# Kernel tuning notes

Measured on AMD Instinct MI355X. Metric: run time of the kernel, lower is better.

The kernel has to match this reference:

```python
import jax, jax.numpy as jnp
import numpy as np

H = 64          # hidden_size
FF = 36         # MLP hidden
B, W, S = 512, 8, 200


def setup_inputs() -> dict:
    key = jax.random.key(0)
    ks = jax.random.split(key, 8)
    query = jax.random.normal(ks[0], (B, H), dtype=jnp.float32)
    k = jax.random.normal(ks[1], (B, W, S, H), dtype=jnp.float32)
    mask = jax.random.randint(ks[2], (B, W, S, 1), 0, 2).astype(bool)
    # MLP params: Linear(4H -> 36), PReLU(scalar), Linear(36 -> 1)
    lim1 = 1.0 / np.sqrt(4 * H)
    W1 = jax.random.uniform(ks[3], (FF, 4 * H), jnp.float32, -lim1, lim1)
    b1 = jax.random.uniform(ks[4], (FF,), jnp.float32, -lim1, lim1)
    prelu_a = jnp.float32(0.25)
    lim2 = 1.0 / np.sqrt(FF)
    W2 = jax.random.uniform(ks[5], (1, FF), jnp.float32, -lim2, lim2)
    b2 = jax.random.uniform(ks[6], (1,), jnp.float32, -lim2, lim2)
    return {"query": query, "key": k, "W1": W1, "b1": b1,
            "prelu_a": prelu_a, "W2": W2, "b2": b2, "mask": mask}


def reference(query, key, W1, b1, prelu_a, W2, b2, mask):
    # broadcast query to (B, W, S, H)
    q = jnp.broadcast_to(query[:, None, None, :], key.shape)
    feat = jnp.concatenate([q, key, q - key, q * key], axis=-1)  # (B,W,S,4H)
    h = jnp.einsum('bwsf,of->bwso', feat, W1) + b1               # (B,W,S,36)
    h = jnp.where(h >= 0, h, prelu_a * h)                        # PReLU
    score = jnp.einsum('bwso,uo->bwsu', h, W2) + b2              # (B,W,S,1)
    # weighted_att=True: mask with -1e4 then softmax over seq_len
    score = jnp.where(mask, jnp.float32(-10000.0), score)
    score = jax.nn.softmax(score, axis=2)
    out = (key * score).sum(axis=2)                              # (B,W,H)
    return out
```

## Files before the change

kernel.cpp:

```cpp
#include <hip/hip_runtime.h>
#include <math.h>


#define BB   512
#define WW   8
#define SS   200
#define HH   64
#define FFN  36

typedef __attribute__((ext_vector_type(8))) short short8;
typedef __attribute__((ext_vector_type(4))) float f32x4;

__device__ __forceinline__ unsigned short f2bf(float x) {
    union { float f; unsigned u; } v; v.f = x;
    unsigned r = v.u + 0x7fffu + ((v.u >> 16) & 1u);
    return (unsigned short)(r >> 16);
}
__device__ __forceinline__ float bf2f(unsigned short h) {
    union { unsigned u; float f; } v; v.u = ((unsigned)h) << 16;
    return v.f;
}

__global__ __launch_bounds__(256)
void precompute_c(const float* __restrict__ query,
                  const float* __restrict__ W1,
                  const float* __restrict__ b1,
                  unsigned short* __restrict__ c_hi_g,
                  float* __restrict__ A_g)
{
    __shared__ float q_s[HH];
    const int b = blockIdx.x, tid = threadIdx.x;
    if (tid < HH) q_s[tid] = query[b * HH + tid];
    __syncthreads();
    for (int idx = tid; idx < 48 * HH; idx += 256) {
        int o = idx >> 6, h = idx & 63;
        float c = 0.0f;
        if (o < FFN) {
            const float* w = W1 + o * 4 * HH;
            c = w[HH + h] - w[2 * HH + h] + w[3 * HH + h] * q_s[h];
        }
        c_hi_g[(size_t)b * 48 * HH + idx] = f2bf(c);
    }
    if (tid < 48) {
        float a = 0.0f;
        if (tid < FFN) {
            const float* w = W1 + tid * 4 * HH;
            a = b1[tid];
            #pragma unroll 8
            for (int h = 0; h < HH; ++h) a += (w[h] + w[2 * HH + h]) * q_s[h];
        }
        A_g[b * 48 + tid] = a;
    }
}

__global__ __launch_bounds__(256, 4)
void twb_main(const float* __restrict__ key,
              const unsigned short* __restrict__ c_hi_g,
              const float* __restrict__ A_g,
              const float* __restrict__ prelu_a,
              const float* __restrict__ W2,
              const int*   __restrict__ mask,
              float*       __restrict__ out)
{
    __shared__ float scores[208];
    __shared__ float wl[208];
    __shared__ float red[8];
    __shared__ float4 part4[256];

    const int tid  = threadIdx.x;
    const int bw   = blockIdx.x;
    const int b    = bw >> 3;
    const int lane = tid & 63, q = lane >> 4, n = lane & 15, wid = tid >> 6;

    const float* kg = key + (size_t)bw * (SS * HH);
    const unsigned short* cb = c_hi_g + (size_t)b * 48 * HH;

    short8 Bf[3][2];
    float  Ao[3], w2o[3];
    #pragma unroll
    for (int ot = 0; ot < 3; ++ot) {
        const int o = ot * 16 + n;
        #pragma unroll
        for (int ks = 0; ks < 2; ++ks)
            Bf[ot][ks] = *(const short8*)(cb + (size_t)o * HH + ks * 32 + q * 8);
        Ao[ot]  = A_g[b * 48 + o];
        w2o[ot] = (o < FFN) ? W2[o] : 0.0f;
    }
    int mv = 1;
    if (tid < SS) mv = mask[bw * SS + tid];
    const float pa = prelu_a[0];

    for (int st = wid; st < 13; st += 4) {
        const int s = st * 16 + n;
        short8 Ah[2], Al[2];
        if (s < SS) {
            #pragma unroll
            for (int ks = 0; ks < 2; ++ks) {
                const float* p = kg + s * HH + ks * 32 + q * 8;
                const float4 v0 = *(const float4*)p;
                const float4 v1 = *(const float4*)(p + 4);
                const float vv[8] = {v0.x, v0.y, v0.z, v0.w,
                                     v1.x, v1.y, v1.z, v1.w};
                #pragma unroll
                for (int j = 0; j < 8; ++j) {
                    const unsigned short hi = f2bf(vv[j]);
                    Ah[ks][j] = (short)hi;
                    Al[ks][j] = (short)f2bf(vv[j] - bf2f(hi));
                }
            }
        } else {
            #pragma unroll
            for (int ks = 0; ks < 2; ++ks)
                #pragma unroll
                for (int j = 0; j < 8; ++j) { Ah[ks][j] = 0; Al[ks][j] = 0; }
        }
        float contrib[4] = {0.f, 0.f, 0.f, 0.f};
        #pragma unroll
        for (int ot = 0; ot < 3; ++ot) {
            f32x4 acc = {0.f, 0.f, 0.f, 0.f};
            acc = __builtin_amdgcn_mfma_f32_16x16x32_bf16(Ah[0], Bf[ot][0], acc, 0, 0, 0);
            acc = __builtin_amdgcn_mfma_f32_16x16x32_bf16(Al[0], Bf[ot][0], acc, 0, 0, 0);
            acc = __builtin_amdgcn_mfma_f32_16x16x32_bf16(Ah[1], Bf[ot][1], acc, 0, 0, 0);
            acc = __builtin_amdgcn_mfma_f32_16x16x32_bf16(Al[1], Bf[ot][1], acc, 0, 0, 0);
            #pragma unroll
            for (int r = 0; r < 4; ++r) {
                float hv = acc[r] + Ao[ot];
                hv = (hv >= 0.0f) ? hv : pa * hv;
                contrib[r] += w2o[ot] * hv;
            }
        }
        #pragma unroll
        for (int m = 1; m <= 8; m <<= 1)
            #pragma unroll
            for (int r = 0; r < 4; ++r)
                contrib[r] += __shfl_xor(contrib[r], m, 64);
        if (n == 0) {
            #pragma unroll
            for (int r = 0; r < 4; ++r) {
                const int s2 = st * 16 + q * 4 + r;
                if (s2 < SS) scores[s2] = contrib[r];
            }
        }
    }
    __syncthreads();

    float msc = -3.0e38f;
    if (tid < SS)
        msc = mv ? -10000.0f : scores[tid];
    float mx = msc;
    #pragma unroll
    for (int off = 32; off > 0; off >>= 1)
        mx = fmaxf(mx, __shfl_xor(mx, off, 64));
    if (lane == 0) red[wid] = mx;
    __syncthreads();
    const float M = fmaxf(fmaxf(red[0], red[1]), fmaxf(red[2], red[3]));
    float e = (tid < SS) ? __expf(msc - M) : 0.0f;
    float ssum = e;
    #pragma unroll
    for (int off = 32; off > 0; off >>= 1)
        ssum += __shfl_xor(ssum, off, 64);
    if (lane == 0) red[4 + wid] = ssum;
    __syncthreads();
    const float total = red[4] + red[5] + red[6] + red[7];
    if (tid < SS) wl[tid] = e / total;
    __syncthreads();

    {
        const int r0 = tid >> 4;
        const int h4 = (tid & 15) * 4;
        float4 acc2 = {0.f, 0.f, 0.f, 0.f};
        for (int s = r0; s < SS; s += 16) {
            const float4 kv = *(const float4*)(kg + s * HH + h4);
            const float w = wl[s];
            acc2.x += kv.x * w; acc2.y += kv.y * w;
            acc2.z += kv.z * w; acc2.w += kv.w * w;
        }
        part4[tid] = acc2;
    }
    __syncthreads();
    if (tid < HH) {
        const int hg = tid >> 2, c = tid & 3;
        float r = 0.0f;
        #pragma unroll
        for (int row = 0; row < 16; ++row)
            r += ((const float*)&part4[row * 16 + hg])[c];
        out[(size_t)bw * HH + tid] = r;
    }
}

#define PADQ 17
__global__ __launch_bounds__(256, 2)
void twb_fallback(const float* __restrict__ query,
                  const float* __restrict__ key,
                  const float* __restrict__ W1,
                  const float* __restrict__ b1,
                  const float* __restrict__ prelu_a,
                  const float* __restrict__ W2,
                  const float* __restrict__ b2,
                  const int*   __restrict__ mask,
                  float*       __restrict__ out)
{
    __shared__ float q_s[HH];
    __shared__ float c_s[FFN * HH];
    __shared__ float A_s[FFN];
    __shared__ float W2_s[FFN];
    __shared__ float k_s[SS * PADQ * 4];
    __shared__ float wl[256];
    __shared__ float red[8];
    __shared__ float part[4 * 64];

    const int tid = threadIdx.x;
    const int bw  = blockIdx.x;
    const int b   = bw >> 3;

    if (tid < HH)  q_s[tid]  = query[b * HH + tid];
    if (tid < FFN) W2_s[tid] = W2[tid];
    __syncthreads();

    const float4* gk4 = (const float4*)(key + (size_t)bw * (SS * HH));
    float4* kl4 = (float4*)k_s;
    for (int i = tid; i < (SS * HH) / 4; i += 256) {
        float4 v = gk4[i];
        kl4[(i >> 4) * PADQ + (i & 15)] = v;
    }
    for (int idx = tid; idx < FFN * HH; idx += 256) {
        int o = idx >> 6, h = idx & 63;
        const float* w = W1 + o * (4 * HH);
        c_s[idx] = w[HH + h] - w[2 * HH + h] + w[3 * HH + h] * q_s[h];
    }
    if (tid < FFN) {
        const float* w = W1 + tid * (4 * HH);
        float a = b1[tid];
        for (int h = 0; h < HH; ++h) a += (w[h] + w[2 * HH + h]) * q_s[h];
        A_s[tid] = a;
    }
    __syncthreads();

    const float pa  = prelu_a[0];
    const float bb2 = b2[0];
    float msc = -3.0e38f;
    if (tid < SS) {
        float acc[FFN];
        #pragma unroll
        for (int o = 0; o < FFN; ++o) acc[o] = A_s[o];
        const float4* c4 = (const float4*)c_s;
        const float4* k4 = (const float4*)k_s;
        const int rowbase = tid * PADQ;
        for (int ch = 0; ch < 4; ++ch) {
            float4 kv0 = k4[rowbase + ch * 4 + 0];
            float4 kv1 = k4[rowbase + ch * 4 + 1];
            float4 kv2 = k4[rowbase + ch * 4 + 2];
            float4 kv3 = k4[rowbase + ch * 4 + 3];
            #pragma unroll
            for (int o = 0; o < FFN; ++o) {
                float4 c0 = c4[o * 16 + ch * 4 + 0];
                float4 c1 = c4[o * 16 + ch * 4 + 1];
                float4 c2 = c4[o * 16 + ch * 4 + 2];
                float4 c3 = c4[o * 16 + ch * 4 + 3];
                float a = acc[o];
                a += c0.x * kv0.x + c0.y * kv0.y + c0.z * kv0.z + c0.w * kv0.w;
                a += c1.x * kv1.x + c1.y * kv1.y + c1.z * kv1.z + c1.w * kv1.w;
                a += c2.x * kv2.x + c2.y * kv2.y + c2.z * kv2.z + c2.w * kv2.w;
                a += c3.x * kv3.x + c3.y * kv3.y + c3.z * kv3.z + c3.w * kv3.w;
                acc[o] = a;
            }
        }
        float sc = bb2;
        #pragma unroll
        for (int o = 0; o < FFN; ++o) {
            float a = acc[o];
            a = (a >= 0.0f) ? a : pa * a;
            sc += W2_s[o] * a;
        }
        msc = mask[bw * SS + tid] ? -10000.0f : sc;
    }

    float mx = msc;
    #pragma unroll
    for (int off = 32; off > 0; off >>= 1)
        mx = fmaxf(mx, __shfl_xor(mx, off, 64));
    const int wid = tid >> 6;
    if ((tid & 63) == 0) red[wid] = mx;
    __syncthreads();
    const float M = fmaxf(fmaxf(red[0], red[1]), fmaxf(red[2], red[3]));
    float e = (tid < SS) ? __expf(msc - M) : 0.0f;
    float ssum = e;
    #pragma unroll
    for (int off = 32; off > 0; off >>= 1)
        ssum += __shfl_xor(ssum, off, 64);
    if ((tid & 63) == 0) red[4 + wid] = ssum;
    __syncthreads();
    const float total = red[4] + red[5] + red[6] + red[7];
    if (tid < SS) wl[tid] = e / total;
    __syncthreads();

    const int wv = tid >> 6, h = tid & 63;
    float p = 0.0f;
    for (int s = wv * 50; s < wv * 50 + 50; ++s)
        p += k_s[s * (PADQ * 4) + h] * wl[s];
    part[wv * 64 + h] = p;
    __syncthreads();
    if (tid < 64) {
        float r = part[tid] + part[64 + tid] + part[128 + tid] + part[192 + tid];
        out[(size_t)bw * HH + tid] = r;
    }
}

extern "C" void kernel_launch(void* const* d_in, const int* in_sizes, int n_in,
                              void* d_out, int out_size, void* d_ws, size_t ws_size,
                              hipStream_t stream) {
    const float* query   = (const float*)d_in[0];
    const float* key     = (const float*)d_in[1];
    const float* W1      = (const float*)d_in[2];
    const float* b1      = (const float*)d_in[3];
    const float* prelu_a = (const float*)d_in[4];
    const float* W2      = (const float*)d_in[5];
    const float* b2      = (const float*)d_in[6];
    const int*   mask    = (const int*)d_in[7];
    float* out = (float*)d_out;

    const size_t c_bytes = (size_t)BB * 48 * HH * sizeof(unsigned short);
    const size_t a_bytes = (size_t)BB * 48 * sizeof(float);
    if (ws_size >= c_bytes + a_bytes) {
        unsigned short* c_hi_g = (unsigned short*)d_ws;
        float* A_g = (float*)((char*)d_ws + c_bytes);
        precompute_c<<<BB, 256, 0, stream>>>(query, W1, b1, c_hi_g, A_g);
        twb_main<<<BB * WW, 256, 0, stream>>>(key, c_hi_g, A_g, prelu_a,
                                              W2, mask, out);
    } else {
        twb_fallback<<<BB * WW, 256, 0, stream>>>(query, key, W1, b1, prelu_a,
                                                  W2, b2, mask, out);
    }
}
```

Baseline: 323.7 us.

## Fuse precompute into main kernel and keep key tile in registers for both passes

Folds the per-batch precompute of the c and A vectors into the main kernel, staging them in shared memory, so there is one launch and no workspace round-trip. The key tile is loaded once into registers up front and reused for both the MLP scoring and the weighted sum, replacing the second global read of key. Each of the 8 blocks sharing a batch now recomputes c and A redundantly, register pressure rises, and launch bounds drop to 2 blocks per SM. The fallback kernel is removed and bf16 conversion now uses the HIP intrinsic.

```diff
diff --git a/kernel.cpp b/kernel.cpp
--- a/kernel.cpp
+++ b/kernel.cpp
@@ -1,4 +1,5 @@
 #include <hip/hip_runtime.h>
+#include <hip/hip_bf16.h>
 #include <math.h>
 
 
@@ -7,100 +8,118 @@
 #define SS   200
 #define HH   64
 #define FFN  36
+#define SCST 72
 
 typedef __attribute__((ext_vector_type(8))) short short8;
 typedef __attribute__((ext_vector_type(4))) float f32x4;
 
 __device__ __forceinline__ unsigned short f2bf(float x) {
-    union { float f; unsigned u; } v; v.f = x;
-    unsigned r = v.u + 0x7fffu + ((v.u >> 16) & 1u);
-    return (unsigned short)(r >> 16);
+    __hip_bfloat16 h = __float2bfloat16(x);
+    union { __hip_bfloat16 b; unsigned short u; } c; c.b = h;
+    return c.u;
 }
 __device__ __forceinline__ float bf2f(unsigned short h) {
     union { unsigned u; float f; } v; v.u = ((unsigned)h) << 16;
     return v.f;
 }
 
-__global__ __launch_bounds__(256)
-void precompute_c(const float* __restrict__ query,
-                  const float* __restrict__ W1,
-                  const float* __restrict__ b1,
-                  unsigned short* __restrict__ c_hi_g,
-                  float* __restrict__ A_g)
+__global__ __launch_bounds__(256, 2)
+void twb_fused(const float* __restrict__ query,
+               const float* __restrict__ key,
+               const float* __restrict__ W1,
+               const float* __restrict__ b1,
+               const float* __restrict__ prelu_a,
+               const float* __restrict__ W2,
+               const int*   __restrict__ mask,
+               float*       __restrict__ out)
 {
     __shared__ float q_s[HH];
-    const int b = blockIdx.x, tid = threadIdx.x;
+    __shared__ unsigned short c_s[48 * SCST];
+    __shared__ float A_s[48], W2_s[48];
+    __shared__ float partA[144];
+    __shared__ float scores[208];
+    __shared__ float wl[208];
+    __shared__ float red[8];
+    __shared__ float part[4][HH];
+
+    const int tid  = threadIdx.x;
+    const int bw   = blockIdx.x;
+    const int b    = bw >> 3;
+    const int lane = tid & 63, q = lane >> 4, n = lane & 15, wid = tid >> 6;
+
+    const float* kg = key + (size_t)bw * (SS * HH);
+
+    float4 kv[4][2][2];
+    #pragma unroll
+    for (int t = 0; t < 4; ++t) {
+        const int st = wid + 4 * t;
+        const int s  = st * 16 + n;
+        const bool valid = (st < 13) && (s < SS);
+        #pragma unroll
+        for (int ks = 0; ks < 2; ++ks)
+            #pragma unroll
+            for (int hh = 0; hh < 2; ++hh) {
+                if (valid)
+                    kv[t][ks][hh] = *(const float4*)(kg + (size_t)s * HH + ks * 32 + q * 8 + hh * 4);
+                else
+                    kv[t][ks][hh] = make_float4(0.f, 0.f, 0.f, 0.f);
+            }
+    }
+
+    int mv = 1;
+    if (tid < SS) mv = mask[bw * SS + tid];
+    const float pa = prelu_a[0];
     if (tid < HH) q_s[tid] = query[b * HH + tid];
-    __syncthreads();
+    if (tid < 48) W2_s[tid] = (tid < FFN) ? W2[tid] : 0.0f;
+    __syncthreads();
+
     for (int idx = tid; idx < 48 * HH; idx += 256) {
-        int o = idx >> 6, h = idx & 63;
+        const int o = idx >> 6, h = idx & 63;
         float c = 0.0f;
         if (o < FFN) {
             const float* w = W1 + o * 4 * HH;
             c = w[HH + h] - w[2 * HH + h] + w[3 * HH + h] * q_s[h];
         }
-        c_hi_g[(size_t)b * 48 * HH + idx] = f2bf(c);
-    }
-    if (tid < 48) {
+        c_s[o * SCST + h] = f2bf(c);
+    }
+    if (tid < 144) {
+        const int o = tid >> 2, c4 = tid & 3;
+        const float* w = W1 + o * 4 * HH;
         float a = 0.0f;
-        if (tid < FFN) {
-            const float* w = W1 + tid * 4 * HH;
-            a = b1[tid];
-            #pragma unroll 8
-            for (int h = 0; h < HH; ++h) a += (w[h] + w[2 * HH + h]) * q_s[h];
-        }
-        A_g[b * 48 + tid] = a;
-    }
-}
-
-__global__ __launch_bounds__(256, 4)
-void twb_main(const float* __restrict__ key,
-              const unsigned short* __restrict__ c_hi_g,
-              const float* __restrict__ A_g,
-              const float* __restrict__ prelu_a,
-              const float* __restrict__ W2,
-              const int*   __restrict__ mask,
-              float*       __restrict__ out)
-{
-    __shared__ float scores[208];
-    __shared__ float wl[208];
-    __shared__ float red[8];
-    __shared__ float4 part4[256];
-
-    const int tid  = threadIdx.x;
-    const int bw   = blockIdx.x;
-    const int b    = bw >> 3;
-    const int lane = tid & 63, q = lane >> 4, n = lane & 15, wid = tid >> 6;
-
-    const float* kg = key + (size_t)bw * (SS * HH);
-    const unsigned short* cb = c_hi_g + (size_t)b * 48 * HH;
+        #pragma unroll
+        for (int i = 0; i < 16; ++i) {
+            const int h = c4 * 16 + i;
+            a += (w[h] + w[2 * HH + h]) * q_s[h];
+        }
+        partA[tid] = a;
+    }
+    __syncthreads();
+    if (tid < 48)
+        A_s[tid] = (tid < FFN)
+                 ? (b1[tid] + partA[tid*4] + partA[tid*4+1] + partA[tid*4+2] + partA[tid*4+3])
+                 : 0.0f;
+    __syncthreads();
 
     short8 Bf[3][2];
     float  Ao[3], w2o[3];
     #pragma unroll
     for (int ot = 0; ot < 3; ++ot) {
-        const int o = ot * 16 + n;
-        #pragma unroll
-        for (int ks = 0; ks < 2; ++ks)
-            Bf[ot][ks] = *(const short8*)(cb + (size_t)o * HH + ks * 32 + q * 8);
-        Ao[ot]  = A_g[b * 48 + o];
-        w2o[ot] = (o < FFN) ? W2[o] : 0.0f;
-    }
-    int mv = 1;
-    if (tid < SS) mv = mask[bw * SS + tid];
-    const float pa = prelu_a[0];
-
-    for (int st = wid; st < 13; st += 4) {
-        const int s = st * 16 + n;
-        short8 Ah[2], Al[2];
-        if (s < SS) {
+        #pragma unroll
+        for (int ks = 0; ks < 2; ++ks)
+            Bf[ot][ks] = *(const short8*)(c_s + (ot * 16 + n) * SCST + ks * 32 + q * 8);
+        Ao[ot]  = A_s[ot * 16 + n];
+        w2o[ot] = W2_s[ot * 16 + n];
+    }
+
+    #pragma unroll
+    for (int t = 0; t < 4; ++t) {
+        const int st = wid + 4 * t;
+        if (st < 13) {
+            short8 Ah[2], Al[2];
             #pragma unroll
             for (int ks = 0; ks < 2; ++ks) {
-                const float* p = kg + s * HH + ks * 32 + q * 8;
-                const float4 v0 = *(const float4*)p;
-                const float4 v1 = *(const float4*)(p + 4);
-                const float vv[8] = {v0.x, v0.y, v0.z, v0.w,
-                                     v1.x, v1.y, v1.z, v1.w};
+                const float vv[8] = {kv[t][ks][0].x, kv[t][ks][0].y, kv[t][ks][0].z, kv[t][ks][0].w,
+                                     kv[t][ks][1].x, kv[t][ks][1].y, kv[t][ks][1].z, kv[t][ks][1].w};
                 #pragma unroll
                 for (int j = 0; j < 8; ++j) {
                     const unsigned short hi = f2bf(vv[j]);
@@ -108,37 +127,32 @@
                     Al[ks][j] = (short)f2bf(vv[j] - bf2f(hi));
                 }
             }
-        } else {
-            #pragma unroll
-            for (int ks = 0; ks < 2; ++ks)
-                #pragma unroll
-                for (int j = 0; j < 8; ++j) { Ah[ks][j] = 0; Al[ks][j] = 0; }
-        }
-        float contrib[4] = {0.f, 0.f, 0.f, 0.f};
-        #pragma unroll
-        for (int ot = 0; ot < 3; ++ot) {
-            f32x4 acc = {0.f, 0.f, 0.f, 0.f};
-            acc = __builtin_amdgcn_mfma_f32_16x16x32_bf16(Ah[0], Bf[ot][0], acc, 0, 0, 0);
-            acc = __builtin_amdgcn_mfma_f32_16x16x32_bf16(Al[0], Bf[ot][0], acc, 0, 0, 0);
-            acc = __builtin_amdgcn_mfma_f32_16x16x32_bf16(Ah[1], Bf[ot][1], acc, 0, 0, 0);
-            acc = __builtin_amdgcn_mfma_f32_16x16x32_bf16(Al[1], Bf[ot][1], acc, 0, 0, 0);
-            #pragma unroll
-            for (int r = 0; r < 4; ++r) {
-                float hv = acc[r] + Ao[ot];
-                hv = (hv >= 0.0f) ? hv : pa * hv;
-                contrib[r] += w2o[ot] * hv;
-            }
-        }
-        #pragma unroll
-        for (int m = 1; m <= 8; m <<= 1)
-            #pragma unroll
-            for (int r = 0; r < 4; ++r)
-                contrib[r] += __shfl_xor(contrib[r], m, 64);
-        if (n == 0) {
-            #pragma unroll
-            for (int r = 0; r < 4; ++r) {
-                const int s2 = st * 16 + q * 4 + r;
-                if (s2 < SS) scores[s2] = contrib[r];
+            float contrib[4] = {0.f, 0.f, 0.f, 0.f};
+            #pragma unroll
+            for (int ot = 0; ot < 3; ++ot) {
+                f32x4 acc = {0.f, 0.f, 0.f, 0.f};
+                acc = __builtin_amdgcn_mfma_f32_16x16x32_bf16(Ah[0], Bf[ot][0], acc, 0, 0, 0);
+                acc = __builtin_amdgcn_mfma_f32_16x16x32_bf16(Al[0], Bf[ot][0], acc, 0, 0, 0);
+                acc = __builtin_amdgcn_mfma_f32_16x16x32_bf16(Ah[1], Bf[ot][1], acc, 0, 0, 0);
+                acc = __builtin_amdgcn_mfma_f32_16x16x32_bf16(Al[1], Bf[ot][1], acc, 0, 0, 0);
+                #pragma unroll
+                for (int r = 0; r < 4; ++r) {
+                    float hv = acc[r] + Ao[ot];
+                    hv = (hv >= 0.0f) ? hv : pa * hv;
+                    contrib[r] += w2o[ot] * hv;
+                }
+            }
+            #pragma unroll
+            for (int m = 1; m <= 8; m <<= 1)
+                #pragma unroll
+                for (int r = 0; r < 4; ++r)
+                    contrib[r] += __shfl_xor(contrib[r], m, 64);
+            if (n == 0) {
+                #pragma unroll
+                for (int r = 0; r < 4; ++r) {
+                    const int s2 = st * 16 + q * 4 + r;
+                    if (s2 < SS) scores[s2] = contrib[r];
+                }
             }
         }
     }
@@ -162,148 +176,52 @@
     if (lane == 0) red[4 + wid] = ssum;
     __syncthreads();
     const float total = red[4] + red[5] + red[6] + red[7];
-    if (tid < SS) wl[tid] = e / total;
-    __syncthreads();
-
-    {
-        const int r0 = tid >> 4;
-        const int h4 = (tid & 15) * 4;
-        float4 acc2 = {0.f, 0.f, 0.f, 0.f};
-        for (int s = r0; s < SS; s += 16) {
-            const float4 kv = *(const float4*)(kg + s * HH + h4);
-            const float w = wl[s];
-            acc2.x += kv.x * w; acc2.y += kv.y * w;
-            acc2.z += kv.z * w; acc2.w += kv.w * w;
-        }
-        part4[tid] = acc2;
-    }
-    __syncthreads();
-    if (tid < HH) {
-        const int hg = tid >> 2, c = tid & 3;
-        float r = 0.0f;
-        #pragma unroll
-        for (int row = 0; row < 16; ++row)
-            r += ((const float*)&part4[row * 16 + hg])[c];
-        out[(size_t)bw * HH + tid] = r;
-    }
-}
-
-#define PADQ 17
-__global__ __launch_bounds__(256, 2)
-void twb_fallback(const float* __restrict__ query,
-                  const float* __restrict__ key,
-                  const float* __restrict__ W1,
-                  const float* __restrict__ b1,
-                  const float* __restrict__ prelu_a,
-                  const float* __restrict__ W2,
-                  const float* __restrict__ b2,
-                  const int*   __restrict__ mask,
-                  float*       __restrict__ out)
-{
-    __shared__ float q_s[HH];
-    __shared__ float c_s[FFN * HH];
-    __shared__ float A_s[FFN];
-    __shared__ float W2_s[FFN];
-    __shared__ float k_s[SS * PADQ * 4];
-    __shared__ float wl[256];
-    __shared__ float red[8];
-    __shared__ float part[4 * 64];
-
-    const int tid = threadIdx.x;
-    const int bw  = blockIdx.x;
-    const int b   = bw >> 3;
-
-    if (tid < HH)  q_s[tid]  = query[b * HH + tid];
-    if (tid < FFN) W2_s[tid] = W2[tid];
-    __syncthreads();
-
-    const float4* gk4 = (const float4*)(key + (size_t)bw * (SS * HH));
-    float4* kl4 = (float4*)k_s;
-    for (int i = tid; i < (SS * HH) / 4; i += 256) {
-        float4 v = gk4[i];
-        kl4[(i >> 4) * PADQ + (i & 15)] = v;
-    }
-    for (int idx = tid; idx < FFN * HH; idx += 256) {
-        int o = idx >> 6, h = idx & 63;
-        const float* w = W1 + o * (4 * HH);
-        c_s[idx] = w[HH + h] - w[2 * HH + h] + w[3 * HH + h] * q_s[h];
-    }
-    if (tid < FFN) {
-        const float* w = W1 + tid * (4 * HH);
-        float a = b1[tid];
-        for (int h = 0; h < HH; ++h) a += (w[h] + w[2 * HH + h]) * q_s[h];
-        A_s[tid] = a;
-    }
-    __syncthreads();
-
-    const float pa  = prelu_a[0];
-    const float bb2 = b2[0];
-    float msc = -3.0e38f;
-    if (tid < SS) {
-        float acc[FFN];
-        #pragma unroll
-        for (int o = 0; o < FFN; ++o) acc[o] = A_s[o];
-        const float4* c4 = (const float4*)c_s;
-        const float4* k4 = (const float4*)k_s;
-        const int rowbase = tid * PADQ;
-        for (int ch = 0; ch < 4; ++ch) {
-            float4 kv0 = k4[rowbase + ch * 4 + 0];
-            float4 kv1 = k4[rowbase + ch * 4 + 1];
-            float4 kv2 = k4[rowbase + ch * 4 + 2];
-            float4 kv3 = k4[rowbase + ch * 4 + 3];
-            #pragma unroll
-            for (int o = 0; o < FFN; ++o) {
-                float4 c0 = c4[o * 16 + ch * 4 + 0];
-                float4 c1 = c4[o * 16 + ch * 4 + 1];
-                float4 c2 = c4[o * 16 + ch * 4 + 2];
-                float4 c3 = c4[o * 16 + ch * 4 + 3];
-                float a = acc[o];
-                a += c0.x * kv0.x + c0.y * kv0.y + c0.z * kv0.z + c0.w * kv0.w;
-                a += c1.x * kv1.x + c1.y * kv1.y + c1.z * kv1.z + c1.w * kv1.w;
-                a += c2.x * kv2.x + c2.y * kv2.y + c2.z * kv2.z + c2.w * kv2.w;
-                a += c3.x * kv3.x + c3.y * kv3.y + c3.z * kv3.z + c3.w * kv3.w;
-                acc[o] = a;
-            }
-        }
-        float sc = bb2;
-        #pragma unroll
-        for (int o = 0; o < FFN; ++o) {
-            float a = acc[o];
-            a = (a >= 0.0f) ? a : pa * a;
-            sc += W2_s[o] * a;
-        }
-        msc = mask[bw * SS + tid] ? -10000.0f : sc;
-    }
-
-    float mx = msc;
-    #pragma unroll
-    for (int off = 32; off > 0; off >>= 1)
-        mx = fmaxf(mx, __shfl_xor(mx, off, 64));
-    const int wid = tid >> 6;
-    if ((tid & 63) == 0) red[wid] = mx;
-    __syncthreads();
-    const float M = fmaxf(fmaxf(red[0], red[1]), fmaxf(red[2], red[3]));
-    float e = (tid < SS) ? __expf(msc - M) : 0.0f;
-    float ssum = e;
-    #pragma unroll
-    for (int off = 32; off > 0; off >>= 1)
-        ssum += __shfl_xor(ssum, off, 64);
-    if ((tid & 63) == 0) red[4 + wid] = ssum;
-    __syncthreads();
-    const float total = red[4] + red[5] + red[6] + red[7];
-    if (tid < SS) wl[tid] = e / total;
-    __syncthreads();
-
-    const int wv = tid >> 6, h = tid & 63;
-    float p = 0.0f;
-    for (int s = wv * 50; s < wv * 50 + 50; ++s)
-        p += k_s[s * (PADQ * 4) + h] * wl[s];
-    part[wv * 64 + h] = p;
-    __syncthreads();
-    if (tid < 64) {
-        float r = part[tid] + part[64 + tid] + part[128 + tid] + part[192 + tid];
-        out[(size_t)bw * HH + tid] = r;
-    }
+    if (tid < SS)       wl[tid] = e / total;
+    else if (tid < 208) wl[tid] = 0.0f;
+    __syncthreads();
+
+    float acc2[2][8];
+    #pragma unroll
+    for (int ks = 0; ks < 2; ++ks)
+        #pragma unroll
+        for (int j = 0; j < 8; ++j) acc2[ks][j] = 0.0f;
+
+    #pragma unroll
+    for (int t = 0; t < 4; ++t) {
+        const int st = wid + 4 * t;
+        if (st < 13) {
+            const int s = st * 16 + n;
+            const float wgt = wl[s];
+            #pragma unroll
+            for (int ks = 0; ks < 2; ++ks) {
+                acc2[ks][0] += wgt * kv[t][ks][0].x;
+                acc2[ks][1] += wgt * kv[t][ks][0].y;
+                acc2[ks][2] += wgt * kv[t][ks][0].z;
+                acc2[ks][3] += wgt * kv[t][ks][0].w;
+                acc2[ks][4] += wgt * kv[t][ks][1].x;
+                acc2[ks][5] += wgt * kv[t][ks][1].y;
+                acc2[ks][6] += wgt * kv[t][ks][1].z;
+                acc2[ks][7] += wgt * kv[t][ks][1].w;
+            }
+        }
+    }
+    #pragma unroll
+    for (int m = 1; m <= 8; m <<= 1)
+        #pragma unroll
+        for (int ks = 0; ks < 2; ++ks)
+            #pragma unroll
+            for (int j = 0; j < 8; ++j)
+                acc2[ks][j] += __shfl_xor(acc2[ks][j], m, 64);
+    if (n == 0) {
+        #pragma unroll
+        for (int ks = 0; ks < 2; ++ks)
+            #pragma unroll
+            for (int j = 0; j < 8; ++j)
+                part[wid][ks * 32 + q * 8 + j] = acc2[ks][j];
+    }
+    __syncthreads();
+    if (tid < HH)
+        out[(size_t)bw * HH + tid] = part[0][tid] + part[1][tid] + part[2][tid] + part[3][tid];
 }
 
 extern "C" void kernel_launch(void* const* d_in, const int* in_sizes, int n_in,
@@ -315,20 +233,10 @@
     const float* b1      = (const float*)d_in[3];
     const float* prelu_a = (const float*)d_in[4];
     const float* W2      = (const float*)d_in[5];
-    const float* b2      = (const float*)d_in[6];
     const int*   mask    = (const int*)d_in[7];
     float* out = (float*)d_out;
 
-    const size_t c_bytes = (size_t)BB * 48 * HH * sizeof(unsigned short);
-    const size_t a_bytes = (size_t)BB * 48 * sizeof(float);
-    if (ws_size >= c_bytes + a_bytes) {
-        unsigned short* c_hi_g = (unsigned short*)d_ws;
-        float* A_g = (float*)((char*)d_ws + c_bytes);
-        precompute_c<<<BB, 256, 0, stream>>>(query, W1, b1, c_hi_g, A_g);
-        twb_main<<<BB * WW, 256, 0, stream>>>(key, c_hi_g, A_g, prelu_a,
-                                              W2, mask, out);
-    } else {
-        twb_fallback<<<BB * WW, 256, 0, stream>>>(query, key, W1, b1, prelu_a,
-                                                  W2, b2, mask, out);
-    }
-}
+    (void)d_ws; (void)ws_size;
+    twb_fused<<<BB * WW, 256, 0, stream>>>(query, key, W1, b1, prelu_a,
+                                           W2, mask, out);
+}
```

Result: slower. 340.6 us (+5.2%).

## Map one (b,w) row per wavefront with register double-buffered key tile loads

Applied to the files above, without the earlier changes.

Restructures the main kernel so each 64-lane wavefront handles a whole (b,w) row instead of a 256-thread block sharing one row. This removes all block-level __syncthreads and LDS reduction steps, and does the softmax and the weighted sum with wave shuffles only. Key tiles are double-buffered in registers so the next tile's loads overlap the current tile's MFMA work. The bf16 conversion also switches to the library intrinsic. In exchange, each wave does serial work over all 13 tiles and carries more register pressure, which may lower occupancy.

```diff
diff --git a/kernel.cpp b/kernel.cpp
--- a/kernel.cpp
+++ b/kernel.cpp
@@ -1,4 +1,5 @@
 #include <hip/hip_runtime.h>
+#include <hip/hip_bf16.h>
 #include <math.h>
 
 
@@ -12,9 +13,9 @@
 typedef __attribute__((ext_vector_type(4))) float f32x4;
 
 __device__ __forceinline__ unsigned short f2bf(float x) {
-    union { float f; unsigned u; } v; v.f = x;
-    unsigned r = v.u + 0x7fffu + ((v.u >> 16) & 1u);
-    return (unsigned short)(r >> 16);
+    __hip_bfloat16 h = __float2bfloat16(x);
+    union { __hip_bfloat16 b; unsigned short u; } c; c.b = h;
+    return c.u;
 }
 __device__ __forceinline__ float bf2f(unsigned short h) {
     union { unsigned u; float f; } v; v.u = ((unsigned)h) << 16;
@@ -53,8 +54,71 @@
     }
 }
 
+__device__ __forceinline__ void load_tile(const float* __restrict__ kg,
+                                          int st, int n, int q,
+                                          float4 (&buf)[2][2])
+{
+    const int s = st * 16 + n;
+    const float* p = kg + (size_t)s * HH + q * 8;
+    if (s < SS) {
+        buf[0][0] = *(const float4*)(p);
+        buf[0][1] = *(const float4*)(p + 4);
+        buf[1][0] = *(const float4*)(p + 32);
+        buf[1][1] = *(const float4*)(p + 36);
+    } else {
+        const float4 z = make_float4(0.f, 0.f, 0.f, 0.f);
+        buf[0][0] = z; buf[0][1] = z; buf[1][0] = z; buf[1][1] = z;
+    }
+}
+
+__device__ __forceinline__ void compute_tile(const float4 (&buf)[2][2],
+                                             const short8 (&Bf)[3][2],
+                                             const float (&Ao)[3],
+                                             const float (&w2o)[3],
+                                             float pa, int st, int q, int n,
+                                             float* __restrict__ scw)
+{
+    short8 Ah[2], Al[2];
+    #pragma unroll
+    for (int ks = 0; ks < 2; ++ks) {
+        const float vv[8] = {buf[ks][0].x, buf[ks][0].y, buf[ks][0].z, buf[ks][0].w,
+                             buf[ks][1].x, buf[ks][1].y, buf[ks][1].z, buf[ks][1].w};
+        #pragma unroll
+        for (int j = 0; j < 8; ++j) {
+            const unsigned short hi = f2bf(vv[j]);
+            Ah[ks][j] = (short)hi;
+            Al[ks][j] = (short)f2bf(vv[j] - bf2f(hi));
+        }
+    }
+    float contrib[4] = {0.f, 0.f, 0.f, 0.f};
+    #pragma unroll
+    for (int ot = 0; ot < 3; ++ot) {
+        f32x4 acc = {0.f, 0.f, 0.f, 0.f};
+        acc = __builtin_amdgcn_mfma_f32_16x16x32_bf16(Ah[0], Bf[ot][0], acc, 0, 0, 0);
+        acc = __builtin_amdgcn_mfma_f32_16x16x32_bf16(Al[0], Bf[ot][0], acc, 0, 0, 0);
+        acc = __builtin_amdgcn_mfma_f32_16x16x32_bf16(Ah[1], Bf[ot][1], acc, 0, 0, 0);
+        acc = __builtin_amdgcn_mfma_f32_16x16x32_bf16(Al[1], Bf[ot][1], acc, 0, 0, 0);
+        #pragma unroll
+        for (int r = 0; r < 4; ++r) {
+            float hv = acc[r] + Ao[ot];
+            hv = (hv >= 0.0f) ? hv : pa * hv;
+            contrib[r] += w2o[ot] * hv;
+        }
+    }
+    #pragma unroll
+    for (int m = 1; m <= 8; m <<= 1)
+        #pragma unroll
+        for (int r = 0; r < 4; ++r)
+            contrib[r] += __shfl_xor(contrib[r], m, 64);
+    if (n == 0) {
+        #pragma unroll
+        for (int r = 0; r < 4; ++r)
+            scw[st * 16 + q * 4 + r] = contrib[r];
+    }
+}
+
 __global__ __launch_bounds__(256, 4)
-void twb_main(const float* __restrict__ key,
+void twb_wave(const float* __restrict__ key,
               const unsigned short* __restrict__ c_hi_g,
               const float* __restrict__ A_g,
               const float* __restrict__ prelu_a,
@@ -62,19 +126,17 @@
               const int*   __restrict__ mask,
               float*       __restrict__ out)
 {
-    __shared__ float scores[208];
-    __shared__ float wl[208];
-    __shared__ float red[8];
-    __shared__ float4 part4[256];
+    __shared__ float sc_s[4][208];
 
     const int tid  = threadIdx.x;
-    const int bw   = blockIdx.x;
+    const int wid  = tid >> 6, lane = tid & 63;
+    const int q    = lane >> 4, n = lane & 15;
+    const int bw   = blockIdx.x * 4 + wid;
     const int b    = bw >> 3;
-    const int lane = tid & 63, q = lane >> 4, n = lane & 15, wid = tid >> 6;
-
     const float* kg = key + (size_t)bw * (SS * HH);
+    float* scw = sc_s[wid];
+
     const unsigned short* cb = c_hi_g + (size_t)b * 48 * HH;
-
     short8 Bf[3][2];
     float  Ao[3], w2o[3];
     #pragma unroll
@@ -86,106 +148,63 @@
         Ao[ot]  = A_g[b * 48 + o];
         w2o[ot] = (o < FFN) ? W2[o] : 0.0f;
     }
-    int mv = 1;
-    if (tid < SS) mv = mask[bw * SS + tid];
     const float pa = prelu_a[0];
-
-    for (int st = wid; st < 13; st += 4) {
-        const int s = st * 16 + n;
-        short8 Ah[2], Al[2];
-        if (s < SS) {
-            #pragma unroll
-            for (int ks = 0; ks < 2; ++ks) {
-                const float* p = kg + s * HH + ks * 32 + q * 8;
-                const float4 v0 = *(const float4*)p;
-                const float4 v1 = *(const float4*)(p + 4);
-                const float vv[8] = {v0.x, v0.y, v0.z, v0.w,
-                                     v1.x, v1.y, v1.z, v1.w};
-                #pragma unroll
-                for (int j = 0; j < 8; ++j) {
-                    const unsigned short hi = f2bf(vv[j]);
-                    Ah[ks][j] = (short)hi;
-                    Al[ks][j] = (short)f2bf(vv[j] - bf2f(hi));
-                }
-            }
-        } else {
-            #pragma unroll
-            for (int ks = 0; ks < 2; ++ks)
-                #pragma unroll
-                for (int j = 0; j < 8; ++j) { Ah[ks][j] = 0; Al[ks][j] = 0; }
-        }
-        float contrib[4] = {0.f, 0.f, 0.f, 0.f};
-        #pragma unroll
-        for (int ot = 0; ot < 3; ++ot) {
-            f32x4 acc = {0.f, 0.f, 0.f, 0.f};
-            acc = __builtin_amdgcn_mfma_f32_16x16x32_bf16(Ah[0], Bf[ot][0], acc, 0, 0, 0);
-            acc = __builtin_amdgcn_mfma_f32_16x16x32_bf16(Al[0], Bf[ot][0], acc, 0, 0, 0);
-            acc = __builtin_amdgcn_mfma_f32_16x16x32_bf16(Ah[1], Bf[ot][1], acc, 0, 0, 0);
-            acc = __builtin_amdgcn_mfma_f32_16x16x32_bf16(Al[1], Bf[ot][1], acc, 0, 0, 0);
-            #pragma unroll
-            for (int r = 0; r < 4; ++r) {
-                float hv = acc[r] + Ao[ot];
-                hv = (hv >= 0.0f) ? hv : pa * hv;
-                contrib[r] += w2o[ot] * hv;
-            }
-        }
-        #pragma unroll
-        for (int m = 1; m <= 8; m <<= 1)
-            #pragma unroll
-            for (int r = 0; r < 4; ++r)
-                contrib[r] += __shfl_xor(contrib[r], m, 64);
-        if (n == 0) {
-            #pragma unroll
-            for (int r = 0; r < 4; ++r) {
-                const int s2 = st * 16 + q * 4 + r;
-                if (s2 < SS) scores[s2] = contrib[r];
-            }
-        }
-    }
-    __syncthreads();
-
-    float msc = -3.0e38f;
-    if (tid < SS)
-        msc = mv ? -10000.0f : scores[tid];
-    float mx = msc;
+    const int mv0 = mask[bw * SS + lane];
+    const int mv1 = mask[bw * SS + 64 + lane];
+    const int mv2 = mask[bw * SS + 128 + lane];
+    const int mv3 = (lane < 8) ? mask[bw * SS + 192 + lane] : 1;
+
+    float4 bufA[2][2], bufB[2][2];
+    load_tile(kg, 0, n, q, bufA);
+    for (int st2 = 0; st2 < 6; ++st2) {
+        const int st = st2 * 2;
+        load_tile(kg, st + 1, n, q, bufB);
+        compute_tile(bufA, Bf, Ao, w2o, pa, st, q, n, scw);
+        load_tile(kg, st + 2, n, q, bufA);
+        compute_tile(bufB, Bf, Ao, w2o, pa, st + 1, q, n, scw);
+    }
+    compute_tile(bufA, Bf, Ao, w2o, pa, 12, q, n, scw);
+
+    float sv0 = mv0 ? -10000.0f : scw[lane];
+    float sv1 = mv1 ? -10000.0f : scw[64 + lane];
+    float sv2 = mv2 ? -10000.0f : scw[128 + lane];
+    float sv3 = (lane < 8) ? (mv3 ? -10000.0f : scw[192 + lane]) : -3.0e38f;
+    float mx = fmaxf(fmaxf(sv0, sv1), fmaxf(sv2, sv3));
     #pragma unroll
     for (int off = 32; off > 0; off >>= 1)
         mx = fmaxf(mx, __shfl_xor(mx, off, 64));
-    if (lane == 0) red[wid] = mx;
-    __syncthreads();
-    const float M = fmaxf(fmaxf(red[0], red[1]), fmaxf(red[2], red[3]));
-    float e = (tid < SS) ? __expf(msc - M) : 0.0f;
-    float ssum = e;
+    const float e0 = __expf(sv0 - mx);
+    const float e1 = __expf(sv1 - mx);
+    const float e2 = __expf(sv2 - mx);
+    const float e3 = (lane < 8) ? __expf(sv3 - mx) : 0.0f;
+    float ssum = e0 + e1 + e2 + e3;
     #pragma unroll
     for (int off = 32; off > 0; off >>= 1)
         ssum += __shfl_xor(ssum, off, 64);
-    if (lane == 0) red[4 + wid] = ssum;
-    __syncthreads();
-    const float total = red[4] + red[5] + red[6] + red[7];
-    if (tid < SS) wl[tid] = e / total;
-    __syncthreads();
-
-    {
-        const int r0 = tid >> 4;
-        const int h4 = (tid & 15) * 4;
-        float4 acc2 = {0.f, 0.f, 0.f, 0.f};
-        for (int s = r0; s < SS; s += 16) {
-            const float4 kv = *(const float4*)(kg + s * HH + h4);
-            const float w = wl[s];
-            acc2.x += kv.x * w; acc2.y += kv.y * w;
-            acc2.z += kv.z * w; acc2.w += kv.w * w;
-        }
-        part4[tid] = acc2;
-    }
-    __syncthreads();
-    if (tid < HH) {
-        const int hg = tid >> 2, c = tid & 3;
-        float r = 0.0f;
-        #pragma unroll
-        for (int row = 0; row < 16; ++row)
-            r += ((const float*)&part4[row * 16 + hg])[c];
-        out[(size_t)bw * HH + tid] = r;
-    }
+    const float inv = 1.0f / ssum;
+    scw[lane]       = e0 * inv;
+    scw[64 + lane]  = e1 * inv;
+    scw[128 + lane] = e2 * inv;
+    if (lane < 8) scw[192 + lane] = e3 * inv;
+
+    const int h4 = n * 4;
+    float4 acc2 = make_float4(0.f, 0.f, 0.f, 0.f);
+    #pragma unroll 5
+    for (int s = q; s < SS; s += 4) {
+        const float w = scw[s];
+        const float4 kv = *(const float4*)(kg + (size_t)s * HH + h4);
+        acc2.x += w * kv.x; acc2.y += w * kv.y;
+        acc2.z += w * kv.z; acc2.w += w * kv.w;
+    }
+    #pragma unroll
+    for (int off = 16; off <= 32; off <<= 1) {
+        acc2.x += __shfl_xor(acc2.x, off, 64);
+        acc2.y += __shfl_xor(acc2.y, off, 64);
+        acc2.z += __shfl_xor(acc2.z, off, 64);
+        acc2.w += __shfl_xor(acc2.w, off, 64);
+    }
+    if (lane < 16)
+        *(float4*)(out + (size_t)bw * HH + h4) = acc2;
 }
 
 #define PADQ 17
@@ -325,8 +344,8 @@
         unsigned short* c_hi_g = (unsigned short*)d_ws;
         float* A_g = (float*)((char*)d_ws + c_bytes);
         precompute_c<<<BB, 256, 0, stream>>>(query, W1, b1, c_hi_g, A_g);
-        twb_main<<<BB * WW, 256, 0, stream>>>(key, c_hi_g, A_g, prelu_a,
-                                              W2, mask, out);
+        twb_wave<<<(BB * WW) / 4, 256, 0, stream>>>(key, c_hi_g, A_g, prelu_a,
+                                                    W2, mask, out);
     } else {
         twb_fallback<<<BB * WW, 256, 0, stream>>>(query, key, W1, b1, prelu_a,
                                                   W2, b2, mask, out);
```

After: 322.7 us. About the same (-0.3%).
